# Kernel optimization log

Measured on AMD Instinct MI355X. Metric: run time of the kernel, lower is better.

The kernel has to match this reference:

```python
import jax, jax.numpy as jnp
import numpy as np

N_NODES = 100000
N_EDGES = 1250000
IN_DIM, HID_DIM, OUT_DIM = 128, 64, 64
NUM_LAYERS = 3
EPS = 1e-12  # F.normalize eps


def setup_inputs() -> dict:
    key = jax.random.key(0)
    ks = jax.random.split(key, 10)
    s = 0.05
    x = jax.random.normal(ks[0], (N_NODES, IN_DIM), dtype=jnp.float32)
    edge_index = jax.random.randint(ks[1], (2, N_EDGES), 0, N_NODES, dtype=jnp.int32)
    W1 = jax.random.normal(ks[2], (IN_DIM, HID_DIM), dtype=jnp.float32) * s
    b1 = jax.random.normal(ks[3], (HID_DIM,), dtype=jnp.float32) * s
    Wl = jax.random.normal(ks[4], (NUM_LAYERS, HID_DIM, HID_DIM), dtype=jnp.float32) * s
    bl = jax.random.normal(ks[5], (NUM_LAYERS, HID_DIM), dtype=jnp.float32) * s
    Wr = jax.random.normal(ks[6], (NUM_LAYERS, HID_DIM, HID_DIM), dtype=jnp.float32) * s
    W2 = jax.random.normal(ks[7], (HID_DIM, OUT_DIM), dtype=jnp.float32) * s
    b2 = jax.random.normal(ks[8], (OUT_DIM,), dtype=jnp.float32) * s
    return {"x": x, "edge_index": edge_index, "W1": W1, "b1": b1,
            "Wl": Wl, "bl": bl, "Wr": Wr, "W2": W2, "b2": b2}


def reference(x, edge_index, W1, b1, Wl, bl, Wr, W2, b2):
    n = x.shape[0]
    src, dst = edge_index[0], edge_index[1]
    # in-degree for mean aggregation (zero-degree -> aggregate stays 0)
    deg = jax.ops.segment_sum(jnp.ones_like(dst, dtype=x.dtype), dst, num_segments=n)
    inv_deg = jnp.where(deg > 0, 1.0 / jnp.maximum(deg, 1.0), 0.0)[:, None]  # [n,1]
    h = x @ W1 + b1  # [n, hid]
    for i in range(Wl.shape[0]):
        # gather source features, scatter-mean to destinations
        agg = jax.ops.segment_sum(h[src], dst, num_segments=n) * inv_deg  # [n, hid]
        o = agg @ Wl[i] + bl[i] + h @ Wr[i]
        # row-wise L2 normalize (PyG normalize=True)
        norm = jnp.sqrt(jnp.sum(o * o, axis=-1, keepdims=True))
        o = o / jnp.maximum(norm, EPS)
        h = jax.nn.relu(o)
    return h @ W2 + b2
```

## Files before the change

kernel.cpp:

```cpp
#include <hip/hip_runtime.h>
#include <hip/hip_bf16.h>


#define NT 256
#define BATCH 4096
#define SBCAP 8192

typedef __attribute__((ext_vector_type(8))) short bf16x8;
typedef __attribute__((ext_vector_type(4))) float f32x4;

__device__ __forceinline__ float bfbits2f(unsigned short b) {
    return __uint_as_float(((unsigned)b) << 16);
}
__device__ __forceinline__ unsigned short f2bfbits(float v) {
    __hip_bfloat16 b = __float2bfloat16(v);
    return *reinterpret_cast<unsigned short*>(&b);
}


__global__ __launch_bounds__(NT) void bin1_kernel(const int* __restrict__ src,
    const int* __restrict__ dst, int m, unsigned* __restrict__ gcur,
    unsigned* __restrict__ bins) {
    __shared__ unsigned hist[256];
    __shared__ unsigned gbase[256];
    const int t = threadIdx.x;
    const int base = blockIdx.x * BATCH;
    hist[t] = 0;
    __syncthreads();
    int d[16], s[16];
    const int e0 = base + t * 16;
    const bool full = (base + BATCH) <= m;
    if (full) {
        #pragma unroll
        for (int q = 0; q < 4; ++q) {
            const int4 dv = *(const int4*)&dst[e0 + q * 4];
            const int4 sv = *(const int4*)&src[e0 + q * 4];
            d[q*4+0]=dv.x; d[q*4+1]=dv.y; d[q*4+2]=dv.z; d[q*4+3]=dv.w;
            s[q*4+0]=sv.x; s[q*4+1]=sv.y; s[q*4+2]=sv.z; s[q*4+3]=sv.w;
        }
        #pragma unroll
        for (int q = 0; q < 16; ++q) atomicAdd(&hist[d[q] >> 9], 1u);
    } else {
        #pragma unroll
        for (int q = 0; q < 16; ++q) {
            const int e = e0 + q;
            if (e < m) { d[q] = dst[e]; s[q] = src[e]; atomicAdd(&hist[d[q] >> 9], 1u); }
            else d[q] = -1;
        }
    }
    __syncthreads();
    {
        const unsigned h = hist[t];
        gbase[t] = h ? atomicAdd(&gcur[t], h) : 0u;
        hist[t] = 0;
    }
    __syncthreads();
    if (full) {
        #pragma unroll
        for (int q = 0; q < 16; ++q) {
            const int b = d[q] >> 9;
            const unsigned slot = gbase[b] + atomicAdd(&hist[b], 1u);
            bins[(size_t)b * SBCAP + slot] = ((unsigned)s[q] << 9) | (unsigned)(d[q] & 511);
        }
    } else {
        #pragma unroll
        for (int q = 0; q < 16; ++q) {
            if (d[q] >= 0) {
                const int b = d[q] >> 9;
                const unsigned slot = gbase[b] + atomicAdd(&hist[b], 1u);
                bins[(size_t)b * SBCAP + slot] = ((unsigned)s[q] << 9) | (unsigned)(d[q] & 511);
            }
        }
    }
}

__global__ void sbase_kernel(const unsigned* __restrict__ gcur, unsigned* __restrict__ sbase,
                             int* __restrict__ row_ptr, int n, int nsb, int m) {
    __shared__ unsigned wsum[4];
    const int t = threadIdx.x, lane = t & 63, wid = t >> 6;
    const unsigned v = (t < nsb) ? gcur[t] : 0u;
    unsigned x = v;
    #pragma unroll
    for (int o = 1; o < 64; o <<= 1) {
        const unsigned tt = __shfl_up(x, o, 64);
        if (lane >= o) x += tt;
    }
    if (lane == 63) wsum[wid] = x;
    __syncthreads();
    unsigned woff = 0;
    for (int w = 0; w < wid; ++w) woff += wsum[w];
    if (t < nsb) sbase[t] = woff + x - v;
    if (t == 0) row_ptr[n] = m;
}

__global__ __launch_bounds__(NT) void bin2_kernel(const unsigned* __restrict__ bins,
    const unsigned* __restrict__ gcur, const unsigned* __restrict__ sbase,
    int* __restrict__ row_ptr, int* __restrict__ csr, int n) {
    __shared__ unsigned hist[512];
    __shared__ unsigned off[512];
    __shared__ unsigned cur[512];
    __shared__ unsigned wsum[4];
    const int k = blockIdx.x;
    const int t = threadIdx.x;
    const int lane = t & 63, wid = t >> 6;
    const int cnt = (int)gcur[k];
    const unsigned sb = sbase[k];
    const unsigned* reg = bins + (size_t)k * SBCAP;
    hist[2*t] = 0; hist[2*t+1] = 0;
    __syncthreads();
    for (int i = t; i < cnt; i += NT) atomicAdd(&hist[reg[i] & 511u], 1u);
    __syncthreads();
    const unsigned v0 = hist[2*t], v1 = hist[2*t+1];
    const unsigned ps = v0 + v1;
    unsigned x = ps;
    #pragma unroll
    for (int o = 1; o < 64; o <<= 1) {
        const unsigned tt = __shfl_up(x, o, 64);
        if (lane >= o) x += tt;
    }
    if (lane == 63) wsum[wid] = x;
    __syncthreads();
    unsigned woff = 0;
    for (int w = 0; w < wid; ++w) woff += wsum[w];
    const unsigned excl = woff + x - ps;
    off[2*t] = excl; off[2*t+1] = excl + v0;
    cur[2*t] = 0; cur[2*t+1] = 0;
    const int node = k * 512 + 2 * t;
    if (node < n)     row_ptr[node]     = (int)(sb + excl);
    if (node + 1 < n) row_ptr[node + 1] = (int)(sb + excl + v0);
    __syncthreads();
    for (int i = t; i < cnt; i += NT) {
        const unsigned u = reg[i];
        const unsigned l = u & 511u;
        const unsigned r = atomicAdd(&cur[l], 1u);
        csr[sb + off[l] + r] = (int)(u >> 9);
    }
}


__global__ void wconv_kernel(const float* __restrict__ W1, const float* __restrict__ Wl,
                             const float* __restrict__ Wr, const float* __restrict__ W2,
                             unsigned short* __restrict__ out) {
    int i = blockIdx.x * blockDim.x + threadIdx.x;
    if (i >= 36864) return;
    float v;
    if (i < 8192) {
        const int col = i >> 7, k = i & 127;
        v = W1[k * 64 + col];
    } else if (i < 32768) {
        const int j = i - 8192;
        const int mm = j >> 13, r = j & 8191;
        const int isR = (r >> 12) & 1, q = r & 4095;
        const int col = q >> 6, k = q & 63;
        v = (isR ? Wr : Wl)[mm * 4096 + k * 64 + col];
    } else {
        const int q = i - 32768;
        const int col = q >> 6, k = q & 63;
        v = W2[k * 64 + col];
    }
    out[i] = f2bfbits(v);
}


__global__ __launch_bounds__(NT) void agg_kernel(const unsigned short* __restrict__ h,
    const int* __restrict__ row_ptr, const int* __restrict__ csr,
    unsigned short* __restrict__ aggB, int n) {
    const int t = threadIdx.x;
    const int lane = t & 63;
    const int g = lane >> 4;
    const int c = lane & 15;
    const int gw = (blockIdx.x * NT + t) >> 6;
    const int nw = (gridDim.x * NT) >> 6;
    for (int node = gw; node < n; node += nw) {
        const int rs = row_ptr[node];
        const int re = row_ptr[node + 1];
        float a0 = 0.f, a1 = 0.f, a2 = 0.f, a3 = 0.f;
        int e = rs;
        for (; e + 16 <= re; e += 16) {
            const int s0 = csr[e + g];
            const int s1 = csr[e + 4 + g];
            const int s2 = csr[e + 8 + g];
            const int s3 = csr[e + 12 + g];
            const ushort4 v0 = *(const ushort4*)&h[(size_t)s0 * 64 + c * 4];
            const ushort4 v1 = *(const ushort4*)&h[(size_t)s1 * 64 + c * 4];
            const ushort4 v2 = *(const ushort4*)&h[(size_t)s2 * 64 + c * 4];
            const ushort4 v3 = *(const ushort4*)&h[(size_t)s3 * 64 + c * 4];
            a0 += (bfbits2f(v0.x) + bfbits2f(v1.x)) + (bfbits2f(v2.x) + bfbits2f(v3.x));
            a1 += (bfbits2f(v0.y) + bfbits2f(v1.y)) + (bfbits2f(v2.y) + bfbits2f(v3.y));
            a2 += (bfbits2f(v0.z) + bfbits2f(v1.z)) + (bfbits2f(v2.z) + bfbits2f(v3.z));
            a3 += (bfbits2f(v0.w) + bfbits2f(v1.w)) + (bfbits2f(v2.w) + bfbits2f(v3.w));
        }
        for (; e + 8 <= re; e += 8) {
            const int s0 = csr[e + g];
            const int s1 = csr[e + 4 + g];
            const ushort4 v0 = *(const ushort4*)&h[(size_t)s0 * 64 + c * 4];
            const ushort4 v1 = *(const ushort4*)&h[(size_t)s1 * 64 + c * 4];
            a0 += bfbits2f(v0.x) + bfbits2f(v1.x);
            a1 += bfbits2f(v0.y) + bfbits2f(v1.y);
            a2 += bfbits2f(v0.z) + bfbits2f(v1.z);
            a3 += bfbits2f(v0.w) + bfbits2f(v1.w);
        }
        for (; e + 4 <= re; e += 4) {
            const int s0 = csr[e + g];
            const ushort4 v0 = *(const ushort4*)&h[(size_t)s0 * 64 + c * 4];
            a0 += bfbits2f(v0.x);
            a1 += bfbits2f(v0.y);
            a2 += bfbits2f(v0.z);
            a3 += bfbits2f(v0.w);
        }
        const int r = re - e;
        if (g < r) {
            const int s0 = csr[e + g];
            const ushort4 v0 = *(const ushort4*)&h[(size_t)s0 * 64 + c * 4];
            a0 += bfbits2f(v0.x);
            a1 += bfbits2f(v0.y);
            a2 += bfbits2f(v0.z);
            a3 += bfbits2f(v0.w);
        }
        a0 += __shfl_xor(a0, 16, 64); a0 += __shfl_xor(a0, 32, 64);
        a1 += __shfl_xor(a1, 16, 64); a1 += __shfl_xor(a1, 32, 64);
        a2 += __shfl_xor(a2, 16, 64); a2 += __shfl_xor(a2, 32, 64);
        a3 += __shfl_xor(a3, 16, 64); a3 += __shfl_xor(a3, 32, 64);
        if (g == 0) {
            const float inv = (re > rs) ? (1.0f / (float)(re - rs)) : 0.0f;
            ushort4 o;
            o.x = f2bfbits(a0 * inv);
            o.y = f2bfbits(a1 * inv);
            o.z = f2bfbits(a2 * inv);
            o.w = f2bfbits(a3 * inv);
            *(ushort4*)&aggB[(size_t)node * 64 + c * 4] = o;
        }
    }
}


template<int A1F32>
__global__ __launch_bounds__(NT) void gemm_mfma(
    const float* __restrict__ A1f, const unsigned short* __restrict__ A1b,
    int ldA1, int K1, const unsigned short* __restrict__ W1t,
    const unsigned short* __restrict__ A2b, const unsigned short* __restrict__ W2t,
    const float* __restrict__ bias, float* __restrict__ outF,
    unsigned short* __restrict__ outB, int n, int do_norm) {
    const int t = threadIdx.x;
    const int lane = t & 63;
    const int w = t >> 6;
    const int r16 = lane & 15;
    const int g = lane >> 4;
    const int row0 = blockIdx.x * 128 + w * 32;

    f32x4 acc[2][4];
    #pragma unroll
    for (int i = 0; i < 2; ++i)
        #pragma unroll
        for (int j = 0; j < 4; ++j) {
            acc[i][j][0] = 0.f; acc[i][j][1] = 0.f; acc[i][j][2] = 0.f; acc[i][j][3] = 0.f;
        }

    int ra[2];
    #pragma unroll
    for (int rt = 0; rt < 2; ++rt) {
        int r = row0 + rt * 16 + r16;
        ra[rt] = (r < n) ? r : (n - 1);
    }

    #pragma unroll 1
    for (int kc = 0; kc < K1; kc += 32) {
        bf16x8 af[2];
        #pragma unroll
        for (int rt = 0; rt < 2; ++rt) {
            if (A1F32) {
                const float* p = &A1f[(size_t)ra[rt] * ldA1 + kc + g * 8];
                const float4 f0 = *(const float4*)p;
                const float4 f1 = *(const float4*)(p + 4);
                bf16x8 a;
                a[0] = (short)f2bfbits(f0.x); a[1] = (short)f2bfbits(f0.y);
                a[2] = (short)f2bfbits(f0.z); a[3] = (short)f2bfbits(f0.w);
                a[4] = (short)f2bfbits(f1.x); a[5] = (short)f2bfbits(f1.y);
                a[6] = (short)f2bfbits(f1.z); a[7] = (short)f2bfbits(f1.w);
                af[rt] = a;
            } else {
                af[rt] = *(const bf16x8*)&A1b[(size_t)ra[rt] * ldA1 + kc + g * 8];
            }
        }
        #pragma unroll
        for (int ct = 0; ct < 4; ++ct) {
            const bf16x8 bw = *(const bf16x8*)&W1t[(size_t)(ct * 16 + r16) * K1 + kc + g * 8];
            acc[0][ct] = __builtin_amdgcn_mfma_f32_16x16x32_bf16(af[0], bw, acc[0][ct], 0, 0, 0);
            acc[1][ct] = __builtin_amdgcn_mfma_f32_16x16x32_bf16(af[1], bw, acc[1][ct], 0, 0, 0);
        }
    }
    if (A2b) {
        #pragma unroll 1
        for (int kc = 0; kc < 64; kc += 32) {
            bf16x8 af[2];
            #pragma unroll
            for (int rt = 0; rt < 2; ++rt)
                af[rt] = *(const bf16x8*)&A2b[(size_t)ra[rt] * 64 + kc + g * 8];
            #pragma unroll
            for (int ct = 0; ct < 4; ++ct) {
                const bf16x8 bw = *(const bf16x8*)&W2t[(size_t)(ct * 16 + r16) * 64 + kc + g * 8];
                acc[0][ct] = __builtin_amdgcn_mfma_f32_16x16x32_bf16(af[0], bw, acc[0][ct], 0, 0, 0);
                acc[1][ct] = __builtin_amdgcn_mfma_f32_16x16x32_bf16(af[1], bw, acc[1][ct], 0, 0, 0);
            }
        }
    }

    float bcol[4];
    #pragma unroll
    for (int ct = 0; ct < 4; ++ct) bcol[ct] = bias[ct * 16 + r16];

    #pragma unroll
    for (int rt = 0; rt < 2; ++rt) {
        #pragma unroll
        for (int ct = 0; ct < 4; ++ct)
            #pragma unroll
            for (int reg = 0; reg < 4; ++reg) acc[rt][ct][reg] += bcol[ct];

        if (do_norm) {
            #pragma unroll
            for (int reg = 0; reg < 4; ++reg) {
                float ss = 0.f;
                #pragma unroll
                for (int ct = 0; ct < 4; ++ct) ss += acc[rt][ct][reg] * acc[rt][ct][reg];
                ss += __shfl_xor(ss, 1, 64);
                ss += __shfl_xor(ss, 2, 64);
                ss += __shfl_xor(ss, 4, 64);
                ss += __shfl_xor(ss, 8, 64);
                const float inv = 1.0f / fmaxf(sqrtf(ss), 1e-12f);
                #pragma unroll
                for (int ct = 0; ct < 4; ++ct)
                    acc[rt][ct][reg] = fmaxf(acc[rt][ct][reg] * inv, 0.0f);
            }
        }

        const int rbase = row0 + rt * 16 + g * 4;
        #pragma unroll
        for (int reg = 0; reg < 4; ++reg) {
            const int rr = rbase + reg;
            if (rr < n) {
                if (outB) {
                    #pragma unroll
                    for (int ct = 0; ct < 4; ++ct)
                        outB[(size_t)rr * 64 + ct * 16 + r16] = f2bfbits(acc[rt][ct][reg]);
                } else {
                    #pragma unroll
                    for (int ct = 0; ct < 4; ++ct)
                        outF[(size_t)rr * 64 + ct * 16 + r16] = acc[rt][ct][reg];
                }
            }
        }
    }
}


extern "C" void kernel_launch(void* const* d_in, const int* in_sizes, int n_in,
                              void* d_out, int out_size, void* d_ws, size_t ws_size,
                              hipStream_t stream) {
    const float* x  = (const float*)d_in[0];
    const int*   ei = (const int*)  d_in[1];
    const float* W1 = (const float*)d_in[2];
    const float* b1 = (const float*)d_in[3];
    const float* Wl = (const float*)d_in[4];
    const float* bl = (const float*)d_in[5];
    const float* Wr = (const float*)d_in[6];
    const float* W2 = (const float*)d_in[7];
    const float* b2 = (const float*)d_in[8];
    float* out = (float*)d_out;

    const int n = in_sizes[0] / 128;
    const int m = in_sizes[1] / 2;
    const int* src = ei;
    const int* dst = ei + m;

    const int nsb = (n + 511) >> 9;

    char* ws = (char*)d_ws;
    size_t off = 0;
    auto alloc = [&](size_t bytes) -> void* {
        void* p = ws + off;
        off = (off + bytes + 255) & ~(size_t)255;
        return p;
    };
    unsigned short* aggB    = (unsigned short*)alloc((size_t)n * 64 * 2);
    unsigned short* hbf     = (unsigned short*)alloc((size_t)n * 64 * 2);
    int*            row_ptr = (int*)alloc((size_t)(n + 1) * sizeof(int));
    unsigned*       gcur    = (unsigned*)alloc((size_t)nsb * 4);
    unsigned*       sbase   = (unsigned*)alloc((size_t)(nsb + 1) * 4);
    unsigned*       bins    = (unsigned*)alloc((size_t)nsb * SBCAP * 4);
    int*            csr     = (int*)alloc((size_t)m * 4);
    unsigned short* wt      = (unsigned short*)alloc(36864 * 2);

    const unsigned short* W1t = wt;
    const unsigned short* W2t = wt + 32768;

    hipMemsetAsync(gcur, 0, (size_t)nsb * 4, stream);

    const int nb1 = (m + BATCH - 1) / BATCH;
    const int gtiles = (n + 127) / 128;

    wconv_kernel<<<144, NT, 0, stream>>>(W1, Wl, Wr, W2, wt);

    gemm_mfma<1><<<gtiles, NT, 0, stream>>>(x, nullptr, 128, 128, W1t,
                                            nullptr, nullptr, b1, nullptr, hbf, n, 0);

    bin1_kernel<<<nb1, NT, 0, stream>>>(src, dst, m, gcur, bins);
    sbase_kernel<<<1, 256, 0, stream>>>(gcur, sbase, row_ptr, n, nsb, m);
    bin2_kernel<<<nsb, NT, 0, stream>>>(bins, gcur, sbase, row_ptr, csr, n);

    for (int i = 0; i < 3; ++i) {
        agg_kernel<<<2048, NT, 0, stream>>>(hbf, row_ptr, csr, aggB, n);
        const unsigned short* Wlt = wt + 8192 + (size_t)i * 8192;
        const unsigned short* Wrt = Wlt + 4096;
        gemm_mfma<0><<<gtiles, NT, 0, stream>>>(nullptr, aggB, 64, 64, Wlt,
                                                hbf, Wrt, bl + (size_t)i * 64,
                                                nullptr, hbf, n, 1);
    }
    gemm_mfma<0><<<gtiles, NT, 0, stream>>>(nullptr, hbf, 64, 64, W2t,
                                            nullptr, nullptr, b2, out, nullptr, n, 0);
}
```

Baseline: 227.1 us.

## Fuse neighbor aggregation with SAGE layer GEMM and final projection

```diff
diff --git a/kernel.cpp b/kernel.cpp
--- a/kernel.cpp
+++ b/kernel.cpp
@@ -5,6 +5,7 @@
 #define NT 256
 #define BATCH 4096
 #define SBCAP 8192
+#define ASTRIDE 72
 
 typedef __attribute__((ext_vector_type(8))) short bf16x8;
 typedef __attribute__((ext_vector_type(4))) float f32x4;
@@ -162,16 +163,90 @@
 }
 
 
-__global__ __launch_bounds__(NT) void agg_kernel(const unsigned short* __restrict__ h,
-    const int* __restrict__ row_ptr, const int* __restrict__ csr,
-    unsigned short* __restrict__ aggB, int n) {
+__global__ __launch_bounds__(NT) void lin1_kernel(
+    const float* __restrict__ x, const unsigned short* __restrict__ W1t,
+    const float* __restrict__ b1, unsigned short* __restrict__ hbf, int n) {
     const int t = threadIdx.x;
     const int lane = t & 63;
+    const int w = t >> 6;
+    const int c = lane & 15;
+    const int g = lane >> 4;
+    const int row0 = blockIdx.x * 128 + w * 32;
+
+    f32x4 acc[2][4];
+    #pragma unroll
+    for (int i = 0; i < 2; ++i)
+        #pragma unroll
+        for (int j = 0; j < 4; ++j) { acc[i][j][0]=0.f; acc[i][j][1]=0.f; acc[i][j][2]=0.f; acc[i][j][3]=0.f; }
+
+    int ra[2];
+    #pragma unroll
+    for (int rt = 0; rt < 2; ++rt) {
+        const int r = row0 + rt * 16 + c;
+        ra[rt] = (r < n) ? r : (n - 1);
+    }
+
+    #pragma unroll 1
+    for (int kc = 0; kc < 128; kc += 32) {
+        bf16x8 af[2];
+        #pragma unroll
+        for (int rt = 0; rt < 2; ++rt) {
+            const float* p = &x[(size_t)ra[rt] * 128 + kc + g * 8];
+            const float4 f0 = *(const float4*)p;
+            const float4 f1 = *(const float4*)(p + 4);
+            bf16x8 a;
+            a[0] = (short)f2bfbits(f0.x); a[1] = (short)f2bfbits(f0.y);
+            a[2] = (short)f2bfbits(f0.z); a[3] = (short)f2bfbits(f0.w);
+            a[4] = (short)f2bfbits(f1.x); a[5] = (short)f2bfbits(f1.y);
+            a[6] = (short)f2bfbits(f1.z); a[7] = (short)f2bfbits(f1.w);
+            af[rt] = a;
+        }
+        #pragma unroll
+        for (int ct = 0; ct < 4; ++ct) {
+            const bf16x8 bw = *(const bf16x8*)&W1t[(size_t)(ct * 16 + c) * 128 + kc + g * 8];
+            acc[0][ct] = __builtin_amdgcn_mfma_f32_16x16x32_bf16(af[0], bw, acc[0][ct], 0, 0, 0);
+            acc[1][ct] = __builtin_amdgcn_mfma_f32_16x16x32_bf16(af[1], bw, acc[1][ct], 0, 0, 0);
+        }
+    }
+
+    float bcol[4];
+    #pragma unroll
+    for (int ct = 0; ct < 4; ++ct) bcol[ct] = b1[ct * 16 + c];
+    #pragma unroll
+    for (int rt = 0; rt < 2; ++rt) {
+        const int rbase = row0 + rt * 16 + g * 4;
+        #pragma unroll
+        for (int reg = 0; reg < 4; ++reg) {
+            const int rr = rbase + reg;
+            if (rr < n) {
+                #pragma unroll
+                for (int ct = 0; ct < 4; ++ct)
+                    hbf[(size_t)rr * 64 + ct * 16 + c] = f2bfbits(acc[rt][ct][reg] + bcol[ct]);
+            }
+        }
+    }
+}
+
+
+template<int LAST>
+__global__ __launch_bounds__(NT) void sage_fused(
+    const unsigned short* __restrict__ hin,
+    const int* __restrict__ row_ptr, const int* __restrict__ csr,
+    const unsigned short* __restrict__ Wlt, const unsigned short* __restrict__ Wrt,
+    const float* __restrict__ bl,
+    const unsigned short* __restrict__ W2t, const float* __restrict__ b2,
+    unsigned short* __restrict__ hout, float* __restrict__ out, int n) {
+    __shared__ unsigned short aggS[128][ASTRIDE];
+    const int t = threadIdx.x;
+    const int lane = t & 63;
+    const int w = t >> 6;
     const int g = lane >> 4;
     const int c = lane & 15;
-    const int gw = (blockIdx.x * NT + t) >> 6;
-    const int nw = (gridDim.x * NT) >> 6;
-    for (int node = gw; node < n; node += nw) {
+    const int tile0 = blockIdx.x * 128;
+
+    for (int i = 0; i < 32; ++i) {
+        const int node = tile0 + w * 32 + i;
+        if (node >= n) break;
         const int rs = row_ptr[node];
         const int re = row_ptr[node + 1];
         float a0 = 0.f, a1 = 0.f, a2 = 0.f, a3 = 0.f;
@@ -181,10 +256,10 @@
             const int s1 = csr[e + 4 + g];
             const int s2 = csr[e + 8 + g];
             const int s3 = csr[e + 12 + g];
-            const ushort4 v0 = *(const ushort4*)&h[(size_t)s0 * 64 + c * 4];
-            const ushort4 v1 = *(const ushort4*)&h[(size_t)s1 * 64 + c * 4];
-            const ushort4 v2 = *(const ushort4*)&h[(size_t)s2 * 64 + c * 4];
-            const ushort4 v3 = *(const ushort4*)&h[(size_t)s3 * 64 + c * 4];
+            const ushort4 v0 = *(const ushort4*)&hin[(size_t)s0 * 64 + c * 4];
+            const ushort4 v1 = *(const ushort4*)&hin[(size_t)s1 * 64 + c * 4];
+            const ushort4 v2 = *(const ushort4*)&hin[(size_t)s2 * 64 + c * 4];
+            const ushort4 v3 = *(const ushort4*)&hin[(size_t)s3 * 64 + c * 4];
             a0 += (bfbits2f(v0.x) + bfbits2f(v1.x)) + (bfbits2f(v2.x) + bfbits2f(v3.x));
             a1 += (bfbits2f(v0.y) + bfbits2f(v1.y)) + (bfbits2f(v2.y) + bfbits2f(v3.y));
             a2 += (bfbits2f(v0.z) + bfbits2f(v1.z)) + (bfbits2f(v2.z) + bfbits2f(v3.z));
@@ -193,8 +268,8 @@
         for (; e + 8 <= re; e += 8) {
             const int s0 = csr[e + g];
             const int s1 = csr[e + 4 + g];
-            const ushort4 v0 = *(const ushort4*)&h[(size_t)s0 * 64 + c * 4];
-            const ushort4 v1 = *(const ushort4*)&h[(size_t)s1 * 64 + c * 4];
+            const ushort4 v0 = *(const ushort4*)&hin[(size_t)s0 * 64 + c * 4];
+            const ushort4 v1 = *(const ushort4*)&hin[(size_t)s1 * 64 + c * 4];
             a0 += bfbits2f(v0.x) + bfbits2f(v1.x);
             a1 += bfbits2f(v0.y) + bfbits2f(v1.y);
             a2 += bfbits2f(v0.z) + bfbits2f(v1.z);
@@ -202,20 +277,16 @@
         }
         for (; e + 4 <= re; e += 4) {
             const int s0 = csr[e + g];
-            const ushort4 v0 = *(const ushort4*)&h[(size_t)s0 * 64 + c * 4];
-            a0 += bfbits2f(v0.x);
-            a1 += bfbits2f(v0.y);
-            a2 += bfbits2f(v0.z);
-            a3 += bfbits2f(v0.w);
+            const ushort4 v0 = *(const ushort4*)&hin[(size_t)s0 * 64 + c * 4];
+            a0 += bfbits2f(v0.x); a1 += bfbits2f(v0.y);
+            a2 += bfbits2f(v0.z); a3 += bfbits2f(v0.w);
         }
         const int r = re - e;
         if (g < r) {
             const int s0 = csr[e + g];
-            const ushort4 v0 = *(const ushort4*)&h[(size_t)s0 * 64 + c * 4];
-            a0 += bfbits2f(v0.x);
-            a1 += bfbits2f(v0.y);
-            a2 += bfbits2f(v0.z);
-            a3 += bfbits2f(v0.w);
+            const ushort4 v0 = *(const ushort4*)&hin[(size_t)s0 * 64 + c * 4];
+            a0 += bfbits2f(v0.x); a1 += bfbits2f(v0.y);
+            a2 += bfbits2f(v0.z); a3 += bfbits2f(v0.w);
         }
         a0 += __shfl_xor(a0, 16, 64); a0 += __shfl_xor(a0, 32, 64);
         a1 += __shfl_xor(a1, 16, 64); a1 += __shfl_xor(a1, 32, 64);
@@ -224,128 +295,129 @@
         if (g == 0) {
             const float inv = (re > rs) ? (1.0f / (float)(re - rs)) : 0.0f;
             ushort4 o;
-            o.x = f2bfbits(a0 * inv);
-            o.y = f2bfbits(a1 * inv);
-            o.z = f2bfbits(a2 * inv);
-            o.w = f2bfbits(a3 * inv);
-            *(ushort4*)&aggB[(size_t)node * 64 + c * 4] = o;
-        }
-    }
-}
-
-
-template<int A1F32>
-__global__ __launch_bounds__(NT) void gemm_mfma(
-    const float* __restrict__ A1f, const unsigned short* __restrict__ A1b,
-    int ldA1, int K1, const unsigned short* __restrict__ W1t,
-    const unsigned short* __restrict__ A2b, const unsigned short* __restrict__ W2t,
-    const float* __restrict__ bias, float* __restrict__ outF,
-    unsigned short* __restrict__ outB, int n, int do_norm) {
-    const int t = threadIdx.x;
-    const int lane = t & 63;
-    const int w = t >> 6;
-    const int r16 = lane & 15;
-    const int g = lane >> 4;
-    const int row0 = blockIdx.x * 128 + w * 32;
+            o.x = f2bfbits(a0 * inv); o.y = f2bfbits(a1 * inv);
+            o.z = f2bfbits(a2 * inv); o.w = f2bfbits(a3 * inv);
+            *(ushort4*)&aggS[w * 32 + i][c * 4] = o;
+        }
+    }
+    __syncthreads();
 
     f32x4 acc[2][4];
     #pragma unroll
     for (int i = 0; i < 2; ++i)
         #pragma unroll
-        for (int j = 0; j < 4; ++j) {
-            acc[i][j][0] = 0.f; acc[i][j][1] = 0.f; acc[i][j][2] = 0.f; acc[i][j][3] = 0.f;
-        }
+        for (int j = 0; j < 4; ++j) { acc[i][j][0]=0.f; acc[i][j][1]=0.f; acc[i][j][2]=0.f; acc[i][j][3]=0.f; }
 
     int ra[2];
     #pragma unroll
     for (int rt = 0; rt < 2; ++rt) {
-        int r = row0 + rt * 16 + r16;
+        const int r = tile0 + w * 32 + rt * 16 + c;
         ra[rt] = (r < n) ? r : (n - 1);
     }
 
-    #pragma unroll 1
-    for (int kc = 0; kc < K1; kc += 32) {
-        bf16x8 af[2];
+    #pragma unroll
+    for (int kc = 0; kc < 64; kc += 32) {
+        bf16x8 a1[2], a2[2];
         #pragma unroll
         for (int rt = 0; rt < 2; ++rt) {
-            if (A1F32) {
-                const float* p = &A1f[(size_t)ra[rt] * ldA1 + kc + g * 8];
-                const float4 f0 = *(const float4*)p;
-                const float4 f1 = *(const float4*)(p + 4);
-                bf16x8 a;
-                a[0] = (short)f2bfbits(f0.x); a[1] = (short)f2bfbits(f0.y);
-                a[2] = (short)f2bfbits(f0.z); a[3] = (short)f2bfbits(f0.w);
-                a[4] = (short)f2bfbits(f1.x); a[5] = (short)f2bfbits(f1.y);
-                a[6] = (short)f2bfbits(f1.z); a[7] = (short)f2bfbits(f1.w);
-                af[rt] = a;
-            } else {
-                af[rt] = *(const bf16x8*)&A1b[(size_t)ra[rt] * ldA1 + kc + g * 8];
-            }
+            a1[rt] = *(const bf16x8*)&aggS[w * 32 + rt * 16 + c][kc + g * 8];
+            a2[rt] = *(const bf16x8*)&hin[(size_t)ra[rt] * 64 + kc + g * 8];
         }
         #pragma unroll
         for (int ct = 0; ct < 4; ++ct) {
-            const bf16x8 bw = *(const bf16x8*)&W1t[(size_t)(ct * 16 + r16) * K1 + kc + g * 8];
-            acc[0][ct] = __builtin_amdgcn_mfma_f32_16x16x32_bf16(af[0], bw, acc[0][ct], 0, 0, 0);
-            acc[1][ct] = __builtin_amdgcn_mfma_f32_16x16x32_bf16(af[1], bw, acc[1][ct], 0, 0, 0);
-        }
-    }
-    if (A2b) {
-        #pragma unroll 1
+            const bf16x8 bw1 = *(const bf16x8*)&Wlt[(size_t)(ct * 16 + c) * 64 + kc + g * 8];
+            const bf16x8 bw2 = *(const bf16x8*)&Wrt[(size_t)(ct * 16 + c) * 64 + kc + g * 8];
+            acc[0][ct] = __builtin_amdgcn_mfma_f32_16x16x32_bf16(a1[0], bw1, acc[0][ct], 0, 0, 0);
+            acc[0][ct] = __builtin_amdgcn_mfma_f32_16x16x32_bf16(a2[0], bw2, acc[0][ct], 0, 0, 0);
+            acc[1][ct] = __builtin_amdgcn_mfma_f32_16x16x32_bf16(a1[1], bw1, acc[1][ct], 0, 0, 0);
+            acc[1][ct] = __builtin_amdgcn_mfma_f32_16x16x32_bf16(a2[1], bw2, acc[1][ct], 0, 0, 0);
+        }
+    }
+
+    float bcol[4];
+    #pragma unroll
+    for (int ct = 0; ct < 4; ++ct) bcol[ct] = bl[ct * 16 + c];
+
+    #pragma unroll
+    for (int rt = 0; rt < 2; ++rt) {
+        #pragma unroll
+        for (int ct = 0; ct < 4; ++ct)
+            #pragma unroll
+            for (int reg = 0; reg < 4; ++reg) acc[rt][ct][reg] += bcol[ct];
+        #pragma unroll
+        for (int reg = 0; reg < 4; ++reg) {
+            float ss = 0.f;
+            #pragma unroll
+            for (int ct = 0; ct < 4; ++ct) ss += acc[rt][ct][reg] * acc[rt][ct][reg];
+            ss += __shfl_xor(ss, 1, 64);
+            ss += __shfl_xor(ss, 2, 64);
+            ss += __shfl_xor(ss, 4, 64);
+            ss += __shfl_xor(ss, 8, 64);
+            const float inv = 1.0f / fmaxf(sqrtf(ss), 1e-12f);
+            #pragma unroll
+            for (int ct = 0; ct < 4; ++ct)
+                acc[rt][ct][reg] = fmaxf(acc[rt][ct][reg] * inv, 0.0f);
+        }
+    }
+
+    if (!LAST) {
+        #pragma unroll
+        for (int rt = 0; rt < 2; ++rt) {
+            const int rbase = tile0 + w * 32 + rt * 16 + g * 4;
+            #pragma unroll
+            for (int reg = 0; reg < 4; ++reg) {
+                const int rr = rbase + reg;
+                if (rr < n) {
+                    #pragma unroll
+                    for (int ct = 0; ct < 4; ++ct)
+                        hout[(size_t)rr * 64 + ct * 16 + c] = f2bfbits(acc[rt][ct][reg]);
+                }
+            }
+        }
+    } else {
+        __syncthreads();
+        #pragma unroll
+        for (int rt = 0; rt < 2; ++rt) {
+            #pragma unroll
+            for (int reg = 0; reg < 4; ++reg) {
+                const int lr = w * 32 + rt * 16 + g * 4 + reg;
+                #pragma unroll
+                for (int ct = 0; ct < 4; ++ct)
+                    aggS[lr][ct * 16 + c] = f2bfbits(acc[rt][ct][reg]);
+            }
+        }
+        __syncthreads();
+        f32x4 acc2[2][4];
+        #pragma unroll
+        for (int i = 0; i < 2; ++i)
+            #pragma unroll
+            for (int j = 0; j < 4; ++j) { acc2[i][j][0]=0.f; acc2[i][j][1]=0.f; acc2[i][j][2]=0.f; acc2[i][j][3]=0.f; }
+        #pragma unroll
         for (int kc = 0; kc < 64; kc += 32) {
             bf16x8 af[2];
             #pragma unroll
             for (int rt = 0; rt < 2; ++rt)
-                af[rt] = *(const bf16x8*)&A2b[(size_t)ra[rt] * 64 + kc + g * 8];
+                af[rt] = *(const bf16x8*)&aggS[w * 32 + rt * 16 + c][kc + g * 8];
             #pragma unroll
             for (int ct = 0; ct < 4; ++ct) {
-                const bf16x8 bw = *(const bf16x8*)&W2t[(size_t)(ct * 16 + r16) * 64 + kc + g * 8];
-                acc[0][ct] = __builtin_amdgcn_mfma_f32_16x16x32_bf16(af[0], bw, acc[0][ct], 0, 0, 0);
-                acc[1][ct] = __builtin_amdgcn_mfma_f32_16x16x32_bf16(af[1], bw, acc[1][ct], 0, 0, 0);
-            }
-        }
-    }
-
-    float bcol[4];
-    #pragma unroll
-    for (int ct = 0; ct < 4; ++ct) bcol[ct] = bias[ct * 16 + r16];
-
-    #pragma unroll
-    for (int rt = 0; rt < 2; ++rt) {
-        #pragma unroll
-        for (int ct = 0; ct < 4; ++ct)
-            #pragma unroll
-            for (int reg = 0; reg < 4; ++reg) acc[rt][ct][reg] += bcol[ct];
-
-        if (do_norm) {
+                const bf16x8 bw = *(const bf16x8*)&W2t[(size_t)(ct * 16 + c) * 64 + kc + g * 8];
+                acc2[0][ct] = __builtin_amdgcn_mfma_f32_16x16x32_bf16(af[0], bw, acc2[0][ct], 0, 0, 0);
+                acc2[1][ct] = __builtin_amdgcn_mfma_f32_16x16x32_bf16(af[1], bw, acc2[1][ct], 0, 0, 0);
+            }
+        }
+        float b2c[4];
+        #pragma unroll
+        for (int ct = 0; ct < 4; ++ct) b2c[ct] = b2[ct * 16 + c];
+        #pragma unroll
+        for (int rt = 0; rt < 2; ++rt) {
+            const int rbase = tile0 + w * 32 + rt * 16 + g * 4;
             #pragma unroll
             for (int reg = 0; reg < 4; ++reg) {
-                float ss = 0.f;
-                #pragma unroll
-                for (int ct = 0; ct < 4; ++ct) ss += acc[rt][ct][reg] * acc[rt][ct][reg];
-                ss += __shfl_xor(ss, 1, 64);
-                ss += __shfl_xor(ss, 2, 64);
-                ss += __shfl_xor(ss, 4, 64);
-                ss += __shfl_xor(ss, 8, 64);
-                const float inv = 1.0f / fmaxf(sqrtf(ss), 1e-12f);
-                #pragma unroll
-                for (int ct = 0; ct < 4; ++ct)
-                    acc[rt][ct][reg] = fmaxf(acc[rt][ct][reg] * inv, 0.0f);
-            }
-        }
-
-        const int rbase = row0 + rt * 16 + g * 4;
-        #pragma unroll
-        for (int reg = 0; reg < 4; ++reg) {
-            const int rr = rbase + reg;
-            if (rr < n) {
-                if (outB) {
+                const int rr = rbase + reg;
+                if (rr < n) {
                     #pragma unroll
                     for (int ct = 0; ct < 4; ++ct)
-                        outB[(size_t)rr * 64 + ct * 16 + r16] = f2bfbits(acc[rt][ct][reg]);
-                } else {
-                    #pragma unroll
-                    for (int ct = 0; ct < 4; ++ct)
-                        outF[(size_t)rr * 64 + ct * 16 + r16] = acc[rt][ct][reg];
+                        out[(size_t)rr * 64 + ct * 16 + c] = acc2[rt][ct][reg] + b2c[ct];
                 }
             }
         }
@@ -381,8 +453,8 @@
         off = (off + bytes + 255) & ~(size_t)255;
         return p;
     };
-    unsigned short* aggB    = (unsigned short*)alloc((size_t)n * 64 * 2);
-    unsigned short* hbf     = (unsigned short*)alloc((size_t)n * 64 * 2);
+    unsigned short* hA      = (unsigned short*)alloc((size_t)n * 64 * 2);
+    unsigned short* hB      = (unsigned short*)alloc((size_t)n * 64 * 2);
     int*            row_ptr = (int*)alloc((size_t)(n + 1) * sizeof(int));
     unsigned*       gcur    = (unsigned*)alloc((size_t)nsb * 4);
     unsigned*       sbase   = (unsigned*)alloc((size_t)(nsb + 1) * 4);
@@ -400,21 +472,19 @@
 
     wconv_kernel<<<144, NT, 0, stream>>>(W1, Wl, Wr, W2, wt);
 
-    gemm_mfma<1><<<gtiles, NT, 0, stream>>>(x, nullptr, 128, 128, W1t,
-                                            nullptr, nullptr, b1, nullptr, hbf, n, 0);
+    lin1_kernel<<<gtiles, NT, 0, stream>>>(x, W1t, b1, hA, n);
 
     bin1_kernel<<<nb1, NT, 0, stream>>>(src, dst, m, gcur, bins);
     sbase_kernel<<<1, 256, 0, stream>>>(gcur, sbase, row_ptr, n, nsb, m);
     bin2_kernel<<<nsb, NT, 0, stream>>>(bins, gcur, sbase, row_ptr, csr, n);
 
-    for (int i = 0; i < 3; ++i) {
-        agg_kernel<<<2048, NT, 0, stream>>>(hbf, row_ptr, csr, aggB, n);
-        const unsigned short* Wlt = wt + 8192 + (size_t)i * 8192;
-        const unsigned short* Wrt = Wlt + 4096;
-        gemm_mfma<0><<<gtiles, NT, 0, stream>>>(nullptr, aggB, 64, 64, Wlt,
-                                                hbf, Wrt, bl + (size_t)i * 64,
-                                                nullptr, hbf, n, 1);
-    }
-    gemm_mfma<0><<<gtiles, NT, 0, stream>>>(nullptr, hbf, 64, 64, W2t,
-                                            nullptr, nullptr, b2, out, nullptr, n, 0);
-}
+    sage_fused<0><<<gtiles, NT, 0, stream>>>(hA, row_ptr, csr,
+                                             wt + 8192, wt + 8192 + 4096, bl,
+                                             nullptr, nullptr, hB, nullptr, n);
+    sage_fused<0><<<gtiles, NT, 0, stream>>>(hB, row_ptr, csr,
+                                             wt + 8192 + 8192, wt + 8192 + 8192 + 4096, bl + 64,
+                                             nullptr, nullptr, hA, nullptr, n);
+    sage_fused<1><<<gtiles, NT, 0, stream>>>(hA, row_ptr, csr,
+                                             wt + 8192 + 16384, wt + 8192 + 16384 + 4096, bl + 128,
+                                             W2t, b2, nullptr, out, n);
+}
```

Result: slower. 299.7 us (+32.0%).

## Fuse final projection into last SAGE layer GEMM and widen aggregation loads

Applied to the files above, without the earlier changes.

```diff
diff --git a/kernel.cpp b/kernel.cpp
--- a/kernel.cpp
+++ b/kernel.cpp
@@ -5,8 +5,10 @@
 #define NT 256
 #define BATCH 4096
 #define SBCAP 8192
+#define HSTRIDE 72
 
 typedef __attribute__((ext_vector_type(8))) short bf16x8;
+typedef __attribute__((ext_vector_type(8))) unsigned short u16x8;
 typedef __attribute__((ext_vector_type(4))) float f32x4;
 
 __device__ __forceinline__ float bfbits2f(unsigned short b) {
@@ -167,80 +169,74 @@
     unsigned short* __restrict__ aggB, int n) {
     const int t = threadIdx.x;
     const int lane = t & 63;
-    const int g = lane >> 4;
-    const int c = lane & 15;
+    const int g = lane >> 3;
+    const int c = lane & 7;
     const int gw = (blockIdx.x * NT + t) >> 6;
     const int nw = (gridDim.x * NT) >> 6;
     for (int node = gw; node < n; node += nw) {
         const int rs = row_ptr[node];
         const int re = row_ptr[node + 1];
-        float a0 = 0.f, a1 = 0.f, a2 = 0.f, a3 = 0.f;
+        float a0=0.f,a1=0.f,a2=0.f,a3=0.f,a4=0.f,a5=0.f,a6=0.f,a7=0.f;
         int e = rs;
         for (; e + 16 <= re; e += 16) {
             const int s0 = csr[e + g];
-            const int s1 = csr[e + 4 + g];
-            const int s2 = csr[e + 8 + g];
-            const int s3 = csr[e + 12 + g];
-            const ushort4 v0 = *(const ushort4*)&h[(size_t)s0 * 64 + c * 4];
-            const ushort4 v1 = *(const ushort4*)&h[(size_t)s1 * 64 + c * 4];
-            const ushort4 v2 = *(const ushort4*)&h[(size_t)s2 * 64 + c * 4];
-            const ushort4 v3 = *(const ushort4*)&h[(size_t)s3 * 64 + c * 4];
-            a0 += (bfbits2f(v0.x) + bfbits2f(v1.x)) + (bfbits2f(v2.x) + bfbits2f(v3.x));
-            a1 += (bfbits2f(v0.y) + bfbits2f(v1.y)) + (bfbits2f(v2.y) + bfbits2f(v3.y));
-            a2 += (bfbits2f(v0.z) + bfbits2f(v1.z)) + (bfbits2f(v2.z) + bfbits2f(v3.z));
-            a3 += (bfbits2f(v0.w) + bfbits2f(v1.w)) + (bfbits2f(v2.w) + bfbits2f(v3.w));
+            const int s1 = csr[e + 8 + g];
+            const u16x8 v0 = *(const u16x8*)&h[(size_t)s0 * 64 + c * 8];
+            const u16x8 v1 = *(const u16x8*)&h[(size_t)s1 * 64 + c * 8];
+            a0 += bfbits2f(v0[0]) + bfbits2f(v1[0]);
+            a1 += bfbits2f(v0[1]) + bfbits2f(v1[1]);
+            a2 += bfbits2f(v0[2]) + bfbits2f(v1[2]);
+            a3 += bfbits2f(v0[3]) + bfbits2f(v1[3]);
+            a4 += bfbits2f(v0[4]) + bfbits2f(v1[4]);
+            a5 += bfbits2f(v0[5]) + bfbits2f(v1[5]);
+            a6 += bfbits2f(v0[6]) + bfbits2f(v1[6]);
+            a7 += bfbits2f(v0[7]) + bfbits2f(v1[7]);
         }
         for (; e + 8 <= re; e += 8) {
             const int s0 = csr[e + g];
-            const int s1 = csr[e + 4 + g];
-            const ushort4 v0 = *(const ushort4*)&h[(size_t)s0 * 64 + c * 4];
-            const ushort4 v1 = *(const ushort4*)&h[(size_t)s1 * 64 + c * 4];
-            a0 += bfbits2f(v0.x) + bfbits2f(v1.x);
-            a1 += bfbits2f(v0.y) + bfbits2f(v1.y);
-            a2 += bfbits2f(v0.z) + bfbits2f(v1.z);
-            a3 += bfbits2f(v0.w) + bfbits2f(v1.w);
-        }
-        for (; e + 4 <= re; e += 4) {
-            const int s0 = csr[e + g];
-            const ushort4 v0 = *(const ushort4*)&h[(size_t)s0 * 64 + c * 4];
-            a0 += bfbits2f(v0.x);
-            a1 += bfbits2f(v0.y);
-            a2 += bfbits2f(v0.z);
-            a3 += bfbits2f(v0.w);
+            const u16x8 v0 = *(const u16x8*)&h[(size_t)s0 * 64 + c * 8];
+            a0 += bfbits2f(v0[0]); a1 += bfbits2f(v0[1]);
+            a2 += bfbits2f(v0[2]); a3 += bfbits2f(v0[3]);
+            a4 += bfbits2f(v0[4]); a5 += bfbits2f(v0[5]);
+            a6 += bfbits2f(v0[6]); a7 += bfbits2f(v0[7]);
         }
         const int r = re - e;
         if (g < r) {
             const int s0 = csr[e + g];
-            const ushort4 v0 = *(const ushort4*)&h[(size_t)s0 * 64 + c * 4];
-            a0 += bfbits2f(v0.x);
-            a1 += bfbits2f(v0.y);
-            a2 += bfbits2f(v0.z);
-            a3 += bfbits2f(v0.w);
-        }
-        a0 += __shfl_xor(a0, 16, 64); a0 += __shfl_xor(a0, 32, 64);
-        a1 += __shfl_xor(a1, 16, 64); a1 += __shfl_xor(a1, 32, 64);
-        a2 += __shfl_xor(a2, 16, 64); a2 += __shfl_xor(a2, 32, 64);
-        a3 += __shfl_xor(a3, 16, 64); a3 += __shfl_xor(a3, 32, 64);
+            const u16x8 v0 = *(const u16x8*)&h[(size_t)s0 * 64 + c * 8];
+            a0 += bfbits2f(v0[0]); a1 += bfbits2f(v0[1]);
+            a2 += bfbits2f(v0[2]); a3 += bfbits2f(v0[3]);
+            a4 += bfbits2f(v0[4]); a5 += bfbits2f(v0[5]);
+            a6 += bfbits2f(v0[6]); a7 += bfbits2f(v0[7]);
+        }
+        #pragma unroll
+        for (int o = 8; o < 64; o <<= 1) {
+            a0 += __shfl_xor(a0, o, 64); a1 += __shfl_xor(a1, o, 64);
+            a2 += __shfl_xor(a2, o, 64); a3 += __shfl_xor(a3, o, 64);
+            a4 += __shfl_xor(a4, o, 64); a5 += __shfl_xor(a5, o, 64);
+            a6 += __shfl_xor(a6, o, 64); a7 += __shfl_xor(a7, o, 64);
+        }
         if (g == 0) {
             const float inv = (re > rs) ? (1.0f / (float)(re - rs)) : 0.0f;
-            ushort4 o;
-            o.x = f2bfbits(a0 * inv);
-            o.y = f2bfbits(a1 * inv);
-            o.z = f2bfbits(a2 * inv);
-            o.w = f2bfbits(a3 * inv);
-            *(ushort4*)&aggB[(size_t)node * 64 + c * 4] = o;
-        }
-    }
-}
-
-
-template<int A1F32>
+            u16x8 o;
+            o[0] = f2bfbits(a0 * inv); o[1] = f2bfbits(a1 * inv);
+            o[2] = f2bfbits(a2 * inv); o[3] = f2bfbits(a3 * inv);
+            o[4] = f2bfbits(a4 * inv); o[5] = f2bfbits(a5 * inv);
+            o[6] = f2bfbits(a6 * inv); o[7] = f2bfbits(a7 * inv);
+            *(u16x8*)&aggB[(size_t)node * 64 + c * 8] = o;
+        }
+    }
+}
+
+
+template<int A1F32, int LAST>
 __global__ __launch_bounds__(NT) void gemm_mfma(
     const float* __restrict__ A1f, const unsigned short* __restrict__ A1b,
     int ldA1, int K1, const unsigned short* __restrict__ W1t,
     const unsigned short* __restrict__ A2b, const unsigned short* __restrict__ W2t,
     const float* __restrict__ bias, float* __restrict__ outF,
-    unsigned short* __restrict__ outB, int n, int do_norm) {
+    unsigned short* __restrict__ outB, int n, int do_norm,
+    const unsigned short* __restrict__ W2t2, const float* __restrict__ b2) {
     const int t = threadIdx.x;
     const int lane = t & 63;
     const int w = t >> 6;
@@ -332,20 +328,72 @@
                     acc[rt][ct][reg] = fmaxf(acc[rt][ct][reg] * inv, 0.0f);
             }
         }
-
-        const int rbase = row0 + rt * 16 + g * 4;
-        #pragma unroll
-        for (int reg = 0; reg < 4; ++reg) {
-            const int rr = rbase + reg;
-            if (rr < n) {
-                if (outB) {
+    }
+
+    if constexpr (!LAST) {
+        #pragma unroll
+        for (int rt = 0; rt < 2; ++rt) {
+            const int rbase = row0 + rt * 16 + g * 4;
+            #pragma unroll
+            for (int reg = 0; reg < 4; ++reg) {
+                const int rr = rbase + reg;
+                if (rr < n) {
+                    if (outB) {
+                        #pragma unroll
+                        for (int ct = 0; ct < 4; ++ct)
+                            outB[(size_t)rr * 64 + ct * 16 + r16] = f2bfbits(acc[rt][ct][reg]);
+                    } else {
+                        #pragma unroll
+                        for (int ct = 0; ct < 4; ++ct)
+                            outF[(size_t)rr * 64 + ct * 16 + r16] = acc[rt][ct][reg];
+                    }
+                }
+            }
+        }
+    } else {
+        __shared__ unsigned short h3S[128][HSTRIDE];
+        #pragma unroll
+        for (int rt = 0; rt < 2; ++rt) {
+            #pragma unroll
+            for (int reg = 0; reg < 4; ++reg) {
+                const int lr = w * 32 + rt * 16 + g * 4 + reg;
+                #pragma unroll
+                for (int ct = 0; ct < 4; ++ct)
+                    h3S[lr][ct * 16 + r16] = f2bfbits(acc[rt][ct][reg]);
+            }
+        }
+        __syncthreads();
+        f32x4 acc2[2][4];
+        #pragma unroll
+        for (int i = 0; i < 2; ++i)
+            #pragma unroll
+            for (int j = 0; j < 4; ++j) { acc2[i][j][0]=0.f; acc2[i][j][1]=0.f; acc2[i][j][2]=0.f; acc2[i][j][3]=0.f; }
+        #pragma unroll
+        for (int kc = 0; kc < 64; kc += 32) {
+            bf16x8 af[2];
+            #pragma unroll
+            for (int rt = 0; rt < 2; ++rt)
+                af[rt] = *(const bf16x8*)&h3S[w * 32 + rt * 16 + r16][kc + g * 8];
+            #pragma unroll
+            for (int ct = 0; ct < 4; ++ct) {
+                const bf16x8 bw = *(const bf16x8*)&W2t2[(size_t)(ct * 16 + r16) * 64 + kc + g * 8];
+                acc2[0][ct] = __builtin_amdgcn_mfma_f32_16x16x32_bf16(af[0], bw, acc2[0][ct], 0, 0, 0);
+                acc2[1][ct] = __builtin_amdgcn_mfma_f32_16x16x32_bf16(af[1], bw, acc2[1][ct], 0, 0, 0);
+            }
+        }
+        float b2c[4];
+        #pragma unroll
+        for (int ct = 0; ct < 4; ++ct) b2c[ct] = b2[ct * 16 + r16];
+        #pragma unroll
+        for (int rt = 0; rt < 2; ++rt) {
+            const int rbase = row0 + rt * 16 + g * 4;
+            #pragma unroll
+            for (int reg = 0; reg < 4; ++reg) {
+                const int rr = rbase + reg;
+                if (rr < n) {
                     #pragma unroll
                     for (int ct = 0; ct < 4; ++ct)
-                        outB[(size_t)rr * 64 + ct * 16 + r16] = f2bfbits(acc[rt][ct][reg]);
-                } else {
-                    #pragma unroll
-                    for (int ct = 0; ct < 4; ++ct)
-                        outF[(size_t)rr * 64 + ct * 16 + r16] = acc[rt][ct][reg];
+                        outF[(size_t)rr * 64 + ct * 16 + r16] = acc2[rt][ct][reg] + b2c[ct];
                 }
             }
         }
@@ -400,21 +448,24 @@
 
     wconv_kernel<<<144, NT, 0, stream>>>(W1, Wl, Wr, W2, wt);
 
-    gemm_mfma<1><<<gtiles, NT, 0, stream>>>(x, nullptr, 128, 128, W1t,
-                                            nullptr, nullptr, b1, nullptr, hbf, n, 0);
+    gemm_mfma<1, 0><<<gtiles, NT, 0, stream>>>(x, nullptr, 128, 128, W1t,
+                                               nullptr, nullptr, b1, nullptr, hbf, n, 0,
+                                               nullptr, nullptr);
 
     bin1_kernel<<<nb1, NT, 0, stream>>>(src, dst, m, gcur, bins);
     sbase_kernel<<<1, 256, 0, stream>>>(gcur, sbase, row_ptr, n, nsb, m);
     bin2_kernel<<<nsb, NT, 0, stream>>>(bins, gcur, sbase, row_ptr, csr, n);
 
-    for (int i = 0; i < 3; ++i) {
+    for (int i = 0; i < 2; ++i) {
         agg_kernel<<<2048, NT, 0, stream>>>(hbf, row_ptr, csr, aggB, n);
         const unsigned short* Wlt = wt + 8192 + (size_t)i * 8192;
         const unsigned short* Wrt = Wlt + 4096;
-        gemm_mfma<0><<<gtiles, NT, 0, stream>>>(nullptr, aggB, 64, 64, Wlt,
-                                                hbf, Wrt, bl + (size_t)i * 64,
-                                                nullptr, hbf, n, 1);
-    }
-    gemm_mfma<0><<<gtiles, NT, 0, stream>>>(nullptr, hbf, 64, 64, W2t,
-                                            nullptr, nullptr, b2, out, nullptr, n, 0);
-}
+        gemm_mfma<0, 0><<<gtiles, NT, 0, stream>>>(nullptr, aggB, 64, 64, Wlt,
+                                                   hbf, Wrt, bl + (size_t)i * 64,
+                                                   nullptr, hbf, n, 1, nullptr, nullptr);
+    }
+    agg_kernel<<<2048, NT, 0, stream>>>(hbf, row_ptr, csr, aggB, n);
+    gemm_mfma<0, 1><<<gtiles, NT, 0, stream>>>(nullptr, aggB, 64, 64, wt + 8192 + 16384,
+                                               hbf, wt + 8192 + 16384 + 4096, bl + 128,
+                                               out, nullptr, n, 1, W2t, b2);
+}
```

Result: no change. 223.6 us (-1.5%).
